# Kernel tuning notes

Measured on AMD Instinct MI355X. Metric: run time of the kernel, lower is better.

The kernel has to match this reference:

```python
import jax, jax.numpy as jnp
import numpy as np
from jax import lax

DN = ('NCHW', 'OIHW', 'NCHW')


def convlstm_layer(x_seq, w, b, hidden):
    """x_seq: [B,T,Cin,H,W] -> hidden sequence [B,T,hidden,H,W]."""
    B, T, _, H, W = x_seq.shape
    h0 = jnp.zeros((B, hidden, H, W), x_seq.dtype)
    c0 = jnp.zeros((B, hidden, H, W), x_seq.dtype)

    def step(carry, xt):
        h, c = carry
        conv_in = jnp.concatenate([xt, h], axis=1)  # [B, Cin+hidden, H, W]
        gates = lax.conv_general_dilated(conv_in, w, (1, 1), 'SAME',
                                         dimension_numbers=DN)
        gates = gates + b[None, :, None, None]
        i, f, o, g = jnp.split(gates, 4, axis=1)
        c_new = jax.nn.sigmoid(f) * c + jax.nn.sigmoid(i) * jnp.tanh(g)
        h_new = jax.nn.sigmoid(o) * jnp.tanh(c_new)
        return (h_new, c_new), h_new

    xs = jnp.swapaxes(x_seq, 0, 1)  # [T,B,Cin,H,W]
    _, hs = lax.scan(step, (h0, c0), xs)  # hs: [T,B,hidden,H,W]
    return jnp.swapaxes(hs, 0, 1)


def setup_inputs() -> dict:
    key = jax.random.key(0)
    ks = jax.random.split(key, 7)
    B, T, H, W = 8, 32, 48, 48
    h1, h2 = 64, 32
    x = jax.random.normal(ks[0], (B, T, 1, H, W), jnp.float32)
    # layer 0: in = 1 + 64, out = 4*64
    w0 = jax.random.normal(ks[1], (4 * h1, 1 + h1, 3, 3), jnp.float32) * 0.05
    b0 = jnp.zeros((4 * h1,), jnp.float32)
    # layer 1: in = 64 + 32, out = 4*32
    w1 = jax.random.normal(ks[2], (4 * h2, h1 + h2, 3, 3), jnp.float32) * 0.05
    b1 = jnp.zeros((4 * h2,), jnp.float32)
    # linear head 32 -> 1
    wl = jax.random.normal(ks[3], (1, h2), jnp.float32) * 0.1
    bl = jnp.zeros((1,), jnp.float32)
    return {"x": x, "w0": w0, "b0": b0, "w1": w1, "b1": b1,
            "wl": wl, "bl": bl}


def reference(x, w0, b0, w1, b1, wl, bl):
    out1 = convlstm_layer(x, w0, b0, 64)   # [B,T,64,H,W]
    out2 = convlstm_layer(out1, w1, b1, 32)  # [B,T,32,H,W]
    o = out2[0]                 # batch element 0: [T,32,H,W]
    o = o.reshape(-1, 32)       # [T*H*W, 32] (raw memory regrouping, as in torch .view)
    return o @ wl.T + bl        # [T*H*W, 1]
```

## Files before the change

### kernel.cpp

```cpp
#include <hip/hip_runtime.h>
#include <cmath>

#define HH 48
#define WW 48
#define HWSZ 2304
#define BB 8
#define TT 32
#define PADPX 2688
#define POFF 64
#define NWAVE 77

typedef unsigned short u16;
typedef __attribute__((ext_vector_type(8))) short bf16x8;
typedef __attribute__((ext_vector_type(4))) float f32x4;
typedef __attribute__((ext_vector_type(4))) short s16x4;

__device__ __forceinline__ u16 f2bf(float f) {
    unsigned int u = __float_as_uint(f);
    u = (u + 0x7fffu + ((u >> 16) & 1u)) >> 16;
    return (u16)u;
}
__device__ __forceinline__ float bf2f(u16 s) {
    return __uint_as_float(((unsigned int)s) << 16);
}
__device__ __forceinline__ float sigm(float x) { return 1.f / (1.f + __expf(-x)); }

__global__ void wprep(const float* __restrict__ w0, const float* __restrict__ w1,
                      u16* __restrict__ wf, float* __restrict__ wxf)
{
    const int gid = blockIdx.x * 256 + threadIdx.x;
    if (gid < 504 * 64) {
        const int lane = gid & 63;
        const int f = gid >> 6;
        const int m = lane & 15;
        const int kh = lane >> 4;
        float v[8];
        if (f < 288) {
            const int g = f & 3;
            int r = f >> 2;
            const int tap = r % 9; r /= 9;
            const int cs = r & 1;
            const int hidg = r >> 1;
            const int oc = g * 64 + hidg * 16 + m;
            #pragma unroll
            for (int j = 0; j < 8; ++j) {
                const int ic = cs * 32 + kh * 8 + j + 1;
                v[j] = w0[((size_t)oc * 65 + ic) * 9 + tap];
            }
        } else {
            const int f2 = f - 288;
            const int g = f2 & 3;
            int r = f2 >> 2;
            const int tap = r % 9; r /= 9;
            const int cs = r % 3;
            const int hidg = r / 3;
            const int oc = g * 32 + hidg * 16 + m;
            #pragma unroll
            for (int j = 0; j < 8; ++j) {
                const int ic = cs * 32 + kh * 8 + j;
                v[j] = w1[((size_t)oc * 96 + ic) * 9 + tap];
            }
        }
        u16 o[8] __attribute__((aligned(16)));
        #pragma unroll
        for (int j = 0; j < 8; ++j) o[j] = f2bf(v[j]);
        *(uint4*)(wf + (size_t)gid * 8) = *(const uint4*)o;
    }
    const int wx = gid - 504 * 64;
    if (wx >= 0 && wx < 2304) {
        const int e = wx & 3;
        const int f4 = wx >> 2;
        const int mb = f4 & 15;
        const int tg = f4 >> 4;
        const int g = tg & 3;
        const int tap = tg >> 2;
        const int m = mb * 4 + e;
        wxf[wx] = w0[((size_t)(g * 64 + m) * 65 + 0) * 9 + tap];
    }
}

__global__ void xprep(const float* __restrict__ x, float* __restrict__ xpad)
{
    const int gid = blockIdx.x * 256 + threadIdx.x;
    if (gid >= TT * BB * PADPX) return;
    const int q = gid % PADPX;
    const int tb = gid / PADPX;
    const int b = tb % BB;
    const int t = tb / BB;
    float v = 0.f;
    const int pl = q - POFF;
    if (pl >= 0) {
        const int py = pl / 50, pxx = pl - py * 50;
        if (py >= 1 && py <= 48 && pxx >= 1 && pxx <= 48)
            v = x[((size_t)b * TT + t) * HWSZ + (py - 1) * 48 + (pxx - 1)];
    }
    xpad[gid] = v;
}

__global__ __launch_bounds__(512, 4) void mstep(
    const u16* __restrict__ in_hi,
    u16* __restrict__ out_hi,
    const float* __restrict__ xpad,
    const u16* __restrict__ wf, const float* __restrict__ wxf,
    const float* __restrict__ b0, const float* __restrict__ b1,
    float* __restrict__ cbuf, float* __restrict__ seq_t,
    int t, int doL0, int doL1, int c0z, int c1z)
{
    __shared__ __align__(16) char ldsA[36864];

    const int tid = threadIdx.x;
    const int lane = tid & 63;
    const int wv = tid >> 6;
    const int lid = blockIdx.x;
    const int b = lid & 7;
    const int r = lid >> 3;
    const int unit = r % 6;
    const int pg = r / 6;
    const bool isL0 = unit < 4;
    if (isL0) { if (!doL0) return; } else { if (!doL1) return; }
    const int frag = pg * 8 + wv;
    const bool active = frag < NWAVE;
    const int p0 = (active ? frag : 0) * 32;
    const int hidg = isL0 ? unit : (unit - 4);
    const bool czero = isL0 ? (c0z != 0) : (c1z != 0);

    const int n   = lane & 15;
    const int khb = (lane >> 4) & 1;
    const int ksl = lane >> 5;
    const int mq  = lane >> 4;

    const int slot = (unit * 8 + b) * NWAVE + (active ? frag : 0);
    float* cptr = cbuf + (size_t)slot * 512;
    const f32x4 cp0 = (active && !czero) ? *(const f32x4*)(cptr + lane * 4)
                                         : (f32x4){0.f, 0.f, 0.f, 0.f};
    const f32x4 cp1 = (active && !czero) ? *(const f32x4*)(cptr + 256 + lane * 4)
                                         : (f32x4){0.f, 0.f, 0.f, 0.f};

    const float* bias = isL0 ? b0 : b1;
    const int CHID = isL0 ? 64 : 32;
    f32x4 acc[2][4];
    #pragma unroll
    for (int g = 0; g < 4; ++g) {
        const f32x4 bv = *(const f32x4*)(bias + g * CHID + hidg * 16 + mq * 4);
        acc[0][g] = bv;
        acc[1][g] = bv;
    }

    const size_t base0 = ((size_t)(ksl * 8 + b) * PADPX + POFF + p0 + n) * 16 + khb * 8;
    const size_t bstride = (size_t)2 * 8 * PADPX * 16;

    const int nsl = isL0 ? 2 : 3;
    const char* pa = ldsA + lane * 16;

    for (int sp = 0; sp < nsl; ++sp) {
        const u16* pbh = in_hi + base0 + (size_t)sp * bstride;
        bf16x8 Bc0 = *(const bf16x8*)(pbh + (long)(-51) * 16);
        bf16x8 Bc1 = *(const bf16x8*)(pbh + (long)(-35) * 16);

        if (sp) __syncthreads();
        const u16* asrc = wf + (isL0 ? (size_t)((hidg * 2 + sp) * 36) * 512
                                     : (size_t)(288 + (hidg * 3 + sp) * 36) * 512);
        #pragma unroll
        for (int i = 0; i < 4; ++i) {
            const int u = tid + 512 * i;
            *(uint4*)(ldsA + (size_t)u * 16) = *(const uint4*)(asrc + (size_t)u * 8);
        }
        if (tid < 256) {
            const int u = tid + 2048;
            *(uint4*)(ldsA + (size_t)u * 16) = *(const uint4*)(asrc + (size_t)u * 8);
        }
        __syncthreads();

        #pragma unroll
        for (int tap = 0; tap < 9; ++tap) {
            bf16x8 Bn0, Bn1;
            if (tap < 8) {
                const int tap2 = tap + 1;
                const int toff2 = ((tap2 / 3) - 1) * 50 + (tap2 % 3) - 1;
                Bn0 = *(const bf16x8*)(pbh + (long)toff2 * 16);
                Bn1 = *(const bf16x8*)(pbh + (long)(toff2 + 16) * 16);
            }
            #pragma unroll
            for (int g = 0; g < 4; ++g) {
                const bf16x8 Ah = *(const bf16x8*)(pa + (size_t)(tap * 4 + g) * 1024);
                acc[0][g] = __builtin_amdgcn_mfma_f32_16x16x32_bf16(Ah, Bc0, acc[0][g], 0, 0, 0);
                acc[1][g] = __builtin_amdgcn_mfma_f32_16x16x32_bf16(Ah, Bc1, acc[1][g], 0, 0, 0);
            }
            if (tap < 8) { Bc0 = Bn0; Bc1 = Bn1; }
        }
    }

    if (isL0) {
        const float* xrow = xpad + (size_t)(t * BB + b) * PADPX + POFF + p0 + n;
        #pragma unroll
        for (int tap = 0; tap < 9; ++tap) {
            const int toff = ((tap / 3) - 1) * 50 + (tap % 3) - 1;
            const float xv0 = xrow[toff];
            const float xv1 = xrow[toff + 16];
            #pragma unroll
            for (int g = 0; g < 4; ++g) {
                const f32x4 wvx = *(const f32x4*)(wxf +
                    ((size_t)(tap * 4 + g) * 16 + hidg * 4 + mq) * 4);
                #pragma unroll
                for (int e = 0; e < 4; ++e) {
                    acc[0][g][e] += wvx[e] * xv0;
                    acc[1][g][e] += wvx[e] * xv1;
                }
            }
        }
    }

    if (!active) return;

    #pragma unroll
    for (int tl = 0; tl < 2; ++tl) {
        const f32x4 cp = tl ? cp1 : cp0;
        const int p = p0 + tl * 16 + n;
        const int py = p / 50, pxx = p - py * 50;
        const bool valid = (py >= 1) && (py <= 48) && (pxx >= 1) && (pxx <= 48);
        const int pix = (py - 1) * 48 + (pxx - 1);
        const bool doseq = (!isL0) && (b == 0) && valid;
        f32x4 cn;
        s16x4 sh;
        #pragma unroll
        for (int e = 0; e < 4; ++e) {
            const float i_ = sigm(acc[tl][0][e]);
            const float f_ = sigm(acc[tl][1][e]);
            const float o_ = sigm(acc[tl][2][e]);
            const float g_ = tanhf(acc[tl][3][e]);
            const float cv = f_ * cp[e] + i_ * g_;
            const float hv = o_ * tanhf(cv);
            cn[e] = cv;
            sh[e] = (short)f2bf(hv);
            if (doseq) {
                const int ch = hidg * 16 + mq * 4 + e;
                __builtin_nontemporal_store(hv, seq_t + (size_t)ch * HWSZ + pix);
            }
        }
        *(f32x4*)(cptr + tl * 256 + lane * 4) = cn;
        if (valid) {
            const int kslot = (isL0 ? 0 : 4) + hidg;
            const size_t ob = (((size_t)kslot * 8 + b) * PADPX + POFF + p) * 16 + mq * 4;
            *(s16x4*)(out_hi + ob) = sh;
        }
    }
}

__global__ void head_kernel(const float* __restrict__ seq,
                            const float* __restrict__ wl,
                            const float* __restrict__ bl,
                            float* __restrict__ out, int nk)
{
    __shared__ float wls[32];
    if (threadIdx.x < 32) wls[threadIdx.x] = wl[threadIdx.x];
    __syncthreads();
    int k = blockIdx.x * 256 + threadIdx.x;
    if (k >= nk) return;
    const float4* p = (const float4*)(seq + (size_t)k * 32);
    float s = bl[0];
    #pragma unroll
    for (int q = 0; q < 8; ++q) {
        float4 f = p[q];
        s += f.x * wls[q * 4 + 0] + f.y * wls[q * 4 + 1]
           + f.z * wls[q * 4 + 2] + f.w * wls[q * 4 + 3];
    }
    out[k] = s;
}

extern "C" void kernel_launch(void* const* d_in, const int* in_sizes, int n_in,
                              void* d_out, int out_size, void* d_ws, size_t ws_size,
                              hipStream_t stream)
{
    const float* x  = (const float*)d_in[0];
    const float* w0 = (const float*)d_in[1];
    const float* b0 = (const float*)d_in[2];
    const float* w1 = (const float*)d_in[3];
    const float* b1 = (const float*)d_in[4];
    const float* wl = (const float*)d_in[5];
    const float* bl = (const float*)d_in[6];
    float* out = (float*)d_out;

    char* p = (char*)d_ws;
    auto alloc = [&](size_t bytes) -> char* {
        char* r = p; p += (bytes + 255) & ~(size_t)255; return r;
    };
    const size_t inbytes = (size_t)6 * BB * PADPX * 16 * 2;
    u16* inA_hi = (u16*)alloc(inbytes);
    u16* inB_hi = (u16*)alloc(inbytes);
    const size_t xbytes = (size_t)TT * BB * PADPX * 4;
    float* xpad = (float*)alloc(xbytes);
    u16* wfall  = (u16*)alloc((size_t)504 * 1024);
    float* wxf  = (float*)alloc((size_t)2304 * 4);
    const size_t cbytes = (size_t)6 * BB * NWAVE * 512 * 4;
    float* cbuf = (float*)alloc(cbytes);
    float* seq  = (float*)alloc((size_t)TT * 32 * HWSZ * 4);

    hipMemsetAsync(inA_hi, 0, inbytes, stream);
    hipMemsetAsync(inB_hi, 0, inbytes, stream);

    wprep<<<(504 * 64 + 2304 + 255) / 256, 256, 0, stream>>>(w0, w1, wfall, wxf);
    xprep<<<(TT * BB * PADPX + 255) / 256, 256, 0, stream>>>(x, xpad);

    for (int s = 0; s <= TT; ++s) {
        const u16* cih = (s & 1) ? inB_hi : inA_hi;
        u16* noh = (s & 1) ? inA_hi : inB_hi;
        const int tq = (s >= 1) ? (s - 1) : 0;
        mstep<<<dim3(480), 512, 0, stream>>>(
            cih, noh, xpad, wfall, wxf, b0, b1,
            cbuf, seq + (size_t)tq * 32 * HWSZ,
            (s < TT) ? s : 0, (s < TT) ? 1 : 0, (s >= 1) ? 1 : 0,
            (s == 0) ? 1 : 0, (s == 1) ? 1 : 0);
    }
    head_kernel<<<288, 256, 0, stream>>>(seq, wl, bl, out, 73728);
}
```

Before: 705.6 us.

## Load two weight slices into LDS at once and prewarm cache before recurrence

Doubles the LDS buffer so the first two input-channel slices of weights are loaded in one pass with a single barrier. Their two B-fragment prefetches are issued up front, and only layer 1 reloads for its third slice. Also adds a warm kernel that reads weights, padded input and state buffers once before the timestep loop so later accesses hit the L2/MALL caches. The larger LDS footprint (72KB per block) may lower occupancy relative to the launch bounds of four blocks, and the warm pass adds one extra kernel launch.

```diff
diff --git a/kernel.cpp b/kernel.cpp
--- a/kernel.cpp
+++ b/kernel.cpp
@@ -97,6 +97,22 @@
     xpad[gid] = v;
 }
 
+__global__ __launch_bounds__(256) void warm(
+    const uint4* __restrict__ w, int nw,
+    const uint4* __restrict__ xp, int nx,
+    const uint4* __restrict__ ha, int nha,
+    const uint4* __restrict__ hb, int nhb)
+{
+    const int gid = blockIdx.x * 256 + threadIdx.x;
+    const int stride = gridDim.x * 256;
+    unsigned int s = 0;
+    for (int u = gid; u < nw; u += stride)  { uint4 v = w[u];  s += v.x + v.y + v.z + v.w; }
+    for (int u = gid; u < nx; u += stride)  { uint4 v = xp[u]; s += v.x + v.y + v.z + v.w; }
+    for (int u = gid; u < nha; u += stride) { uint4 v = ha[u]; s += v.x + v.y + v.z + v.w; }
+    for (int u = gid; u < nhb; u += stride) { uint4 v = hb[u]; s += v.x + v.y + v.z + v.w; }
+    asm volatile("" :: "v"(s));
+}
+
 __global__ __launch_bounds__(512, 4) void mstep(
     const u16* __restrict__ in_hi,
     u16* __restrict__ out_hi,
@@ -106,7 +122,7 @@
     float* __restrict__ cbuf, float* __restrict__ seq_t,
     int t, int doL0, int doL1, int c0z, int c1z)
 {
-    __shared__ __align__(16) char ldsA[36864];
+    __shared__ __align__(16) char ldsA[73728];
 
     const int tid = threadIdx.x;
     const int lane = tid & 63;
@@ -149,28 +165,7 @@
     const size_t base0 = ((size_t)(ksl * 8 + b) * PADPX + POFF + p0 + n) * 16 + khb * 8;
     const size_t bstride = (size_t)2 * 8 * PADPX * 16;
 
-    const int nsl = isL0 ? 2 : 3;
-    const char* pa = ldsA + lane * 16;
-
-    for (int sp = 0; sp < nsl; ++sp) {
-        const u16* pbh = in_hi + base0 + (size_t)sp * bstride;
-        bf16x8 Bc0 = *(const bf16x8*)(pbh + (long)(-51) * 16);
-        bf16x8 Bc1 = *(const bf16x8*)(pbh + (long)(-35) * 16);
-
-        if (sp) __syncthreads();
-        const u16* asrc = wf + (isL0 ? (size_t)((hidg * 2 + sp) * 36) * 512
-                                     : (size_t)(288 + (hidg * 3 + sp) * 36) * 512);
-        #pragma unroll
-        for (int i = 0; i < 4; ++i) {
-            const int u = tid + 512 * i;
-            *(uint4*)(ldsA + (size_t)u * 16) = *(const uint4*)(asrc + (size_t)u * 8);
-        }
-        if (tid < 256) {
-            const int u = tid + 2048;
-            *(uint4*)(ldsA + (size_t)u * 16) = *(const uint4*)(asrc + (size_t)u * 8);
-        }
-        __syncthreads();
-
+    auto ctaps = [&](const u16* pbh, const char* paS, bf16x8 Bc0, bf16x8 Bc1) {
         #pragma unroll
         for (int tap = 0; tap < 9; ++tap) {
             bf16x8 Bn0, Bn1;
@@ -182,15 +177,50 @@
             }
             #pragma unroll
             for (int g = 0; g < 4; ++g) {
-                const bf16x8 Ah = *(const bf16x8*)(pa + (size_t)(tap * 4 + g) * 1024);
+                const bf16x8 Ah = *(const bf16x8*)(paS + (size_t)(tap * 4 + g) * 1024);
                 acc[0][g] = __builtin_amdgcn_mfma_f32_16x16x32_bf16(Ah, Bc0, acc[0][g], 0, 0, 0);
                 acc[1][g] = __builtin_amdgcn_mfma_f32_16x16x32_bf16(Ah, Bc1, acc[1][g], 0, 0, 0);
             }
             if (tap < 8) { Bc0 = Bn0; Bc1 = Bn1; }
         }
-    }
-
-    if (isL0) {
+    };
+
+    const u16* pbh0 = in_hi + base0;
+    const u16* pbh1 = in_hi + base0 + bstride;
+    bf16x8 B00 = *(const bf16x8*)(pbh0 + (long)(-51) * 16);
+    bf16x8 B01 = *(const bf16x8*)(pbh0 + (long)(-35) * 16);
+    bf16x8 B10 = *(const bf16x8*)(pbh1 + (long)(-51) * 16);
+    bf16x8 B11 = *(const bf16x8*)(pbh1 + (long)(-35) * 16);
+
+    const u16* agrp = isL0 ? (wf + (size_t)(hidg * 2 * 36) * 512)
+                           : (wf + (size_t)(288 + hidg * 3 * 36) * 512);
+    #pragma unroll
+    for (int i = 0; i < 9; ++i) {
+        const int u = tid + 512 * i;
+        *(uint4*)(ldsA + (size_t)u * 16) = *(const uint4*)(agrp + (size_t)u * 8);
+    }
+    __syncthreads();
+    ctaps(pbh0, ldsA + lane * 16, B00, B01);
+    ctaps(pbh1, ldsA + 36864 + lane * 16, B10, B11);
+
+    if (!isL0) {
+        const u16* pbh2 = in_hi + base0 + 2 * bstride;
+        bf16x8 B20 = *(const bf16x8*)(pbh2 + (long)(-51) * 16);
+        bf16x8 B21 = *(const bf16x8*)(pbh2 + (long)(-35) * 16);
+        __syncthreads();
+        const u16* a2 = wf + (size_t)(288 + (hidg * 3 + 2) * 36) * 512;
+        #pragma unroll
+        for (int i = 0; i < 4; ++i) {
+            const int u = tid + 512 * i;
+            *(uint4*)(ldsA + (size_t)u * 16) = *(const uint4*)(a2 + (size_t)u * 8);
+        }
+        if (tid < 256) {
+            const int u = tid + 2048;
+            *(uint4*)(ldsA + (size_t)u * 16) = *(const uint4*)(a2 + (size_t)u * 8);
+        }
+        __syncthreads();
+        ctaps(pbh2, ldsA + lane * 16, B20, B21);
+    } else {
         const float* xrow = xpad + (size_t)(t * BB + b) * PADPX + POFF + p0 + n;
         #pragma unroll
         for (int tap = 0; tap < 9; ++tap) {
@@ -289,7 +319,8 @@
     u16* inB_hi = (u16*)alloc(inbytes);
     const size_t xbytes = (size_t)TT * BB * PADPX * 4;
     float* xpad = (float*)alloc(xbytes);
-    u16* wfall  = (u16*)alloc((size_t)504 * 1024);
+    const size_t wbytes = (size_t)504 * 1024;
+    u16* wfall  = (u16*)alloc(wbytes);
     float* wxf  = (float*)alloc((size_t)2304 * 4);
     const size_t cbytes = (size_t)6 * BB * NWAVE * 512 * 4;
     float* cbuf = (float*)alloc(cbytes);
@@ -300,6 +331,11 @@
 
     wprep<<<(504 * 64 + 2304 + 255) / 256, 256, 0, stream>>>(w0, w1, wfall, wxf);
     xprep<<<(TT * BB * PADPX + 255) / 256, 256, 0, stream>>>(x, xpad);
+    warm<<<480, 256, 0, stream>>>(
+        (const uint4*)wfall, (int)(wbytes / 16),
+        (const uint4*)xpad, (int)(xbytes / 16),
+        (const uint4*)inA_hi, (int)(inbytes / 16),
+        (const uint4*)inB_hi, (int)(inbytes / 16));
 
     for (int s = 0; s <= TT; ++s) {
         const u16* cih = (s & 1) ? inB_hi : inA_hi;
```

New measurement: 1.971 ms. 2.79x slower.
